# Kernel optimization log

Hardware: AMD Instinct MI355X
Metric: run time of the kernel (lower is better)

## Reference

```python
import jax, jax.numpy as jnp
import numpy as np

EPS = 1.1920929e-07  # torch clamp_probs eps for float32
TEMP = 0.3           # sampler temperature T


def conv1d(x, w, b, pad):
    # x: [B, Cin, L], w: [Cout, Cin, K] -> [B, Cout, L']
    y = jax.lax.conv_general_dilated(x, w, window_strides=(1,), padding=[(pad, pad)],
                                     dimension_numbers=('NCH', 'OIH', 'NCH'))
    return y + b[None, :, None]


def setup_inputs() -> dict:
    key = jax.random.key(0)
    ks = jax.random.split(key, 20)
    B, L, V, E, F, H, K = 512, 512, 100000, 100, 100, 100, 10
    p = lambda i, shape: jax.random.normal(ks[i], shape, jnp.float32) * 0.02
    return {
        'x': jax.random.randint(ks[0], (B, L), 0, V, dtype=jnp.int32),
        'u': jax.random.uniform(ks[1], (B, K, L), dtype=jnp.float32),
        'emb': p(2, (V, E)),
        'conv1_w': p(3, (F, E, 3)), 'conv1_b': p(4, (F,)),
        'gi_w': p(5, (H, F)), 'gi_b': p(6, (H,)),
        'conv2_w': p(7, (H, F, 3)), 'conv2_b': p(8, (H,)),
        'li_w': p(9, (H, H, 3)), 'li_b': p(10, (H,)),
        'conv3_w': p(11, (F, 2 * H, 1)), 'conv3_b': p(12, (F,)),
        'conv4_w': p(13, (1, F, 1)), 'conv4_b': p(14, (1,)),
        'fc1_w': p(15, (H, E)), 'fc1_b': p(16, (H,)),
        'head_w': p(17, (1, H)), 'head_b': p(18, (1,)),
    }


def _ti_logits(e, conv1_w, conv1_b, gi_w, gi_b, conv2_w, conv2_b,
               li_w, li_b, conv3_w, conv3_b, conv4_w, conv4_b):
    relu = jax.nn.relu
    xt = jnp.swapaxes(e, 1, 2)                       # [B, E, L]
    h = relu(conv1d(xt, conv1_w, conv1_b, 1))        # [B, F, L]
    g = relu(h.mean(axis=-1) @ gi_w.T + gi_b)        # [B, H] (AdaptiveAvgPool1d(1))
    loc = relu(conv1d(relu(conv1d(h, conv2_w, conv2_b, 1)), li_w, li_b, 1))  # [B, H, L]
    gexp = jnp.broadcast_to(g[:, :, None], loc.shape)
    z = jnp.concatenate([gexp, loc], axis=1)         # [B, 2H, L]
    z = relu(conv1d(z, conv3_w, conv3_b, 0))
    return conv1d(z, conv4_w, conv4_b, 0)            # [B, 1, L]


def reference(x, u, emb, conv1_w, conv1_b, gi_w, gi_b, conv2_w, conv2_b,
              li_w, li_b, conv3_w, conv3_b, conv4_w, conv4_b,
              fc1_w, fc1_b, head_w, head_b):
    e = emb[x]                                       # [B, L, E] embedding gather
    logits = _ti_logits(e, conv1_w, conv1_b, gi_w, gi_b, conv2_w, conv2_b,
                        li_w, li_b, conv3_w, conv3_b, conv4_w, conv4_b)
    # Gumbel top-k continuous sampling (training path)
    uc = jnp.clip(u, EPS, 1.0 - EPS)
    gumbel = -jnp.log(-jnp.log(uc))                  # [B, K, L]
    noisy = (gumbel + logits) / TEMP                 # logits [B,1,L] broadcasts over K
    csamples = jax.nn.softmax(noisy, axis=-1).max(axis=1)  # [B, L]
    # distil predictor: masked mean pooling + MLP + sigmoid head
    pooled = (e * csamples[:, :, None]).mean(axis=1)  # [B, E]
    h = jax.nn.relu(pooled @ fc1_w.T + fc1_b)
    out = jax.nn.sigmoid(h @ head_w.T + head_b)       # [B, 1]
    return out, csamples
```

## Files before the change

### kernel.cpp

```cpp
#include <hip/hip_runtime.h>
#include <math.h>

#define DEV __device__ __forceinline__

typedef __attribute__((ext_vector_type(8))) short short8;
typedef __attribute__((ext_vector_type(4))) short short4v;
typedef __attribute__((ext_vector_type(4))) float f32x4;

#define SSTR 136

DEV short f2bf(float f) {
    unsigned u = __builtin_bit_cast(unsigned, f);
    unsigned r = (u + 0x7fffu + ((u >> 16) & 1u)) >> 16;
    return (short)r;
}

__global__ __launch_bounds__(64) void pack_all_kernel(
    const float* __restrict__ c1w, const float* __restrict__ c2w,
    const float* __restrict__ liw, const float* __restrict__ c3w,
    short* __restrict__ A1, short* __restrict__ A2,
    short* __restrict__ A3, short* __restrict__ A4) {
    int bx = blockIdx.x;
    const float* w; short* dst; int mode, lbx;
    if (bx < 77)       { w = c1w; dst = A1; mode = 0; lbx = bx; }
    else if (bx < 154) { w = c2w; dst = A2; mode = 0; lbx = bx - 77; }
    else if (bx < 231) { w = liw; dst = A3; mode = 0; lbx = bx - 154; }
    else               { w = c3w; dst = A4; mode = 1; lbx = bx - 231; }
    int ks = lbx / 7, mt = lbx - ks * 7;
    int lane = threadIdx.x;
    int f = mt * 16 + (lane & 15);
    int kb = ks * 32 + (lane >> 4) * 8;
    short8 v;
#pragma unroll
    for (int j = 0; j < 8; ++j) {
        int kk = kb + j;
        float val = 0.f;
        if (f < 100) {
            if (mode == 0) {
                int dk = kk / 112, c = kk - dk * 112;
                if (dk < 3 && c < 100) val = w[(f * 100 + c) * 3 + dk];
            } else {
                if (kk < 100) val = w[f * 200 + 100 + kk];
            }
        }
        v[j] = f2bf(val);
    }
    *(short8*)&dst[(lbx * 64 + lane) * 8] = v;
}

template<int NT, bool POOL, bool TO_GLOBAL>
DEV void conv3tap(const short* __restrict__ Ap, const float* __restrict__ bias,
                  const short* s_src, short* s_dst, short* __restrict__ gout,
                  int row0l, int l0, float* __restrict__ hpart, int pbase,
                  int lane, int wv) {
    const int q = lane >> 4, n = lane & 15;
    const int mt0 = wv * 2;
    const bool two = (wv < 3);
    const f32x4 z4 = {0.f, 0.f, 0.f, 0.f};
    f32x4 acc0[NT], acc1[NT];
#pragma unroll
    for (int nt = 0; nt < NT; ++nt) { acc0[nt] = z4; acc1[nt] = z4; }
#pragma unroll
    for (int ks = 0; ks < 11; ++ks) {
        short8 a0 = *(const short8*)&Ap[(ks * 448 + mt0 * 64 + lane) * 8];
        short8 a1;
        if (two) a1 = *(const short8*)&Ap[(ks * 448 + (mt0 + 1) * 64 + lane) * 8];
        int oct = ks * 4 + q, dk, c0;
        if (oct >= 42) { dk = 0; c0 = 0; }
        else { dk = oct / 14; c0 = (oct - dk * 14) * 8; }
#pragma unroll
        for (int nt = 0; nt < NT; ++nt) {
            int r = nt * 16 + n + dk; if (r > 69) r = 69;
            short8 bf = *(const short8*)&s_src[r * SSTR + c0];
            acc0[nt] = __builtin_amdgcn_mfma_f32_16x16x32_bf16(a0, bf, acc0[nt], 0, 0, 0);
            if (two)
                acc1[nt] = __builtin_amdgcn_mfma_f32_16x16x32_bf16(a1, bf, acc1[nt], 0, 0, 0);
        }
    }
    const int fb0 = mt0 * 16 + q * 4;
    const int fb1 = fb0 + 16;
    f32x4 bs0 = (fb0 < 100) ? *(const f32x4*)&bias[fb0] : z4;
    f32x4 bs1 = (two && fb1 < 100) ? *(const f32x4*)&bias[fb1] : z4;
    f32x4 ps0 = z4, ps1 = z4;
#pragma unroll
    for (int nt = 0; nt < NT; ++nt) {
        const int j = nt * 16 + n;
        const int l = row0l + j;
        const bool lok = (l >= 0) && (l < 512);
        const bool pok = (l >= l0) && (l < l0 + 64);
        short4v pk0, pk1;
#pragma unroll
        for (int r = 0; r < 4; ++r) {
            float v0 = fmaxf(acc0[nt][r] + bs0[r], 0.f);
            v0 = lok ? v0 : 0.f;
            pk0[r] = f2bf(v0);
            if constexpr (POOL) { if (pok) ps0[r] += v0; }
            if (two) {
                float v1 = fmaxf(acc1[nt][r] + bs1[r], 0.f);
                v1 = lok ? v1 : 0.f;
                pk1[r] = f2bf(v1);
                if constexpr (POOL) { if (pok) ps1[r] += v1; }
            }
        }
        if constexpr (TO_GLOBAL) {
            if (j < 64) {
                *(short4v*)&gout[j * 112 + fb0] = pk0;
                if (two) *(short4v*)&gout[j * 112 + fb1] = pk1;
            }
        } else {
            if (j < 70) {
                *(short4v*)&s_dst[j * SSTR + fb0] = pk0;
                if (two) *(short4v*)&s_dst[j * SSTR + fb1] = pk1;
            }
        }
    }
    if constexpr (POOL) {
#pragma unroll
        for (int off = 1; off <= 8; off <<= 1)
#pragma unroll
            for (int r = 0; r < 4; ++r) {
                ps0[r] += __shfl_xor(ps0[r], off, 64);
                ps1[r] += __shfl_xor(ps1[r], off, 64);
            }
        if (n == 0) {
            *(f32x4*)&hpart[pbase * 112 + fb0] = ps0;
            if (two) *(f32x4*)&hpart[pbase * 112 + fb1] = ps1;
        }
    }
}

__global__ __launch_bounds__(256, 4) void fused_conv_kernel(
    const int* __restrict__ xidx, const float* __restrict__ emb,
    const short* __restrict__ A1, const short* __restrict__ A2,
    const short* __restrict__ A3,
    const float* __restrict__ b1, const float* __restrict__ b2,
    const float* __restrict__ b3,
    short* __restrict__ locT, float* __restrict__ hpart) {
    extern __shared__ char smem[];
    short* s_e = (short*)smem;
    short* s_h = (short*)(smem + 72 * SSTR * 2);
    const int tid = threadIdx.x;
    const int b = blockIdx.y, bx = blockIdx.x, l0 = bx * 64;
    const int lane = tid & 63, wv = tid >> 6;

#pragma unroll
    for (int idx = tid; idx < 70 * 28; idx += 256) {
        int j = idx / 28, c4 = idx - j * 28;
        int lg = l0 - 3 + j;
        short4v v = {0, 0, 0, 0};
        if (c4 < 25) {
            if (lg >= 0 && lg < 512) {
                int row = xidx[b * 512 + lg];
                f32x4 ev = *(const f32x4*)&emb[row * 100 + c4 * 4];
#pragma unroll
                for (int r = 0; r < 4; ++r) v[r] = f2bf(ev[r]);
            }
        }
        *(short4v*)&s_e[j * SSTR + c4 * 4] = v;
    }
    __syncthreads();
    conv3tap<5, true, false>(A1, b1, s_e, s_h, nullptr, l0 - 2, l0,
                             hpart, b * 8 + bx, lane, wv);
    __syncthreads();
    conv3tap<5, false, false>(A2, b2, s_h, s_e, nullptr, l0 - 1, l0,
                              nullptr, 0, lane, wv);
    __syncthreads();
    conv3tap<4, false, true>(A3, b3, s_e, nullptr,
                             locT + ((size_t)b * 512 + l0) * 112, l0, l0,
                             nullptr, 0, lane, wv);
}

__global__ __launch_bounds__(256, 4) void conv3_logits_kernel(
    const short* __restrict__ locT, const short* __restrict__ A4,
    const float* __restrict__ zg, const float* __restrict__ w4,
    const float* __restrict__ b4, float* __restrict__ logits) {
    extern __shared__ char smem[];
    short* s_in = (short*)smem;
    float* s_part = (float*)(smem + 128 * SSTR * 2);
    const int tid = threadIdx.x;
    const int b = blockIdx.y, l0r = blockIdx.x * 128;
    const int lane = tid & 63, wv = tid >> 6;
    const int q = lane >> 4, n = lane & 15;

    {
        short8 tmp[7];
#pragma unroll
        for (int p = 0; p < 7; ++p) {
            int idx = tid + p * 256;
            int j = idx / 14, c8 = idx - j * 14;
            tmp[p] = *(const short8*)&locT[((size_t)b * 512 + l0r + j) * 112 + c8 * 8];
        }
#pragma unroll
        for (int p = 0; p < 7; ++p) {
            int idx = tid + p * 256;
            int j = idx / 14, c8 = idx - j * 14;
            *(short8*)&s_in[j * SSTR + c8 * 8] = tmp[p];
        }
    }
    __syncthreads();

    const f32x4 z4 = {0.f, 0.f, 0.f, 0.f};
    const int mt0 = wv * 2;
    const bool two = (wv < 3);
    f32x4 acc0[8], acc1[8];
#pragma unroll
    for (int nt = 0; nt < 8; ++nt) { acc0[nt] = z4; acc1[nt] = z4; }
#pragma unroll
    for (int ks = 0; ks < 4; ++ks) {
        short8 a0 = *(const short8*)&A4[(ks * 448 + mt0 * 64 + lane) * 8];
        short8 a1;
        if (two) a1 = *(const short8*)&A4[(ks * 448 + (mt0 + 1) * 64 + lane) * 8];
        int c0 = (ks * 4 + q) * 8;
        if (c0 > 104) c0 = 104;
#pragma unroll
        for (int nt = 0; nt < 8; ++nt) {
            short8 bf = *(const short8*)&s_in[(nt * 16 + n) * SSTR + c0];
            acc0[nt] = __builtin_amdgcn_mfma_f32_16x16x32_bf16(a0, bf, acc0[nt], 0, 0, 0);
            if (two)
                acc1[nt] = __builtin_amdgcn_mfma_f32_16x16x32_bf16(a1, bf, acc1[nt], 0, 0, 0);
        }
    }
    const int fb0 = mt0 * 16 + q * 4, fb1 = fb0 + 16;
    f32x4 w40 = (fb0 < 100) ? *(const f32x4*)&w4[fb0] : z4;
    f32x4 w41 = (two && fb1 < 100) ? *(const f32x4*)&w4[fb1] : z4;
    f32x4 zg0 = *(const f32x4*)&zg[b * 112 + fb0];
    f32x4 zg1 = two ? *(const f32x4*)&zg[b * 112 + fb1] : z4;
#pragma unroll
    for (int nt = 0; nt < 8; ++nt) {
        float part = 0.f;
#pragma unroll
        for (int r = 0; r < 4; ++r) {
            part += fmaxf(acc0[nt][r] + zg0[r], 0.f) * w40[r];
            if (two) part += fmaxf(acc1[nt][r] + zg1[r], 0.f) * w41[r];
        }
        part += __shfl_xor(part, 16, 64);
        part += __shfl_xor(part, 32, 64);
        if (q == 0) s_part[wv * 128 + nt * 16 + n] = part;
    }
    __syncthreads();
    if (tid < 128) {
        float s = s_part[tid] + s_part[128 + tid] + s_part[256 + tid] +
                  s_part[384 + tid] + b4[0];
        logits[b * 512 + l0r + tid] = s;
    }
}

__global__ __launch_bounds__(128) void pool_gate_kernel(
    const float* __restrict__ hpart, const float* __restrict__ gi_w,
    const float* __restrict__ gi_b, const float* __restrict__ w3,
    const float* __restrict__ b3, float* __restrict__ zg) {
    int b = blockIdx.x, tid = threadIdx.x;
    __shared__ float s_hm[112];
    __shared__ float s_g[100];
    if (tid < 112) {
        float a = 0.f;
#pragma unroll
        for (int s = 0; s < 8; ++s) a += hpart[(b * 8 + s) * 112 + tid];
        s_hm[tid] = a * (1.f / 512.f);
    }
    __syncthreads();
    if (tid < 100) {
        float a = gi_b[tid];
        for (int f = 0; f < 100; ++f) a += s_hm[f] * gi_w[tid * 100 + f];
        s_g[tid] = fmaxf(a, 0.f);
    }
    __syncthreads();
    if (tid < 112) {
        float a = 0.f;
        if (tid < 100) {
            a = b3[tid];
            for (int h = 0; h < 100; ++h) a += s_g[h] * w3[tid * 200 + h];
        }
        zg[b * 112 + tid] = a;
    }
}

__global__ __launch_bounds__(256) void sampler_kernel(
    const float* __restrict__ u, const float* __restrict__ logits,
    float* __restrict__ cs) {
    const float EPSV = 1.1920929e-07f;
    int b = blockIdx.x, tid = threadIdx.x;
    int lane = tid & 63, wv = tid >> 6;
    __shared__ float s_log[512], s_cs[512], s_red[8];
    float uu[20];
#pragma unroll
    for (int k = 0; k < 10; ++k) {
        uu[k * 2]     = u[(b * 10 + k) * 512 + tid];
        uu[k * 2 + 1] = u[(b * 10 + k) * 512 + tid + 256];
    }
    for (int l = tid; l < 512; l += 256) { s_log[l] = logits[b * 512 + l]; s_cs[l] = 0.f; }
    __syncthreads();
    for (int k = 0; k < 10; ++k) {
        float nz[2];
#pragma unroll
        for (int i = 0; i < 2; ++i) {
            int l = tid + i * 256;
            float vv = fminf(fmaxf(uu[k * 2 + i], EPSV), 1.f - EPSV);
            float g = -__logf(-__logf(vv));
            nz[i] = (g + s_log[l]) * (1.f / 0.3f);
        }
        float m = fmaxf(nz[0], nz[1]);
#pragma unroll
        for (int off = 32; off >= 1; off >>= 1) m = fmaxf(m, __shfl_xor(m, off, 64));
        if (lane == 0) s_red[wv] = m;
        __syncthreads();
        m = fmaxf(fmaxf(s_red[0], s_red[1]), fmaxf(s_red[2], s_red[3]));
        float e0 = __expf(nz[0] - m), e1 = __expf(nz[1] - m);
        float s = e0 + e1;
#pragma unroll
        for (int off = 32; off >= 1; off >>= 1) s += __shfl_xor(s, off, 64);
        if (lane == 0) s_red[4 + wv] = s;
        __syncthreads();
        float inv = 1.f / (s_red[4] + s_red[5] + s_red[6] + s_red[7]);
        s_cs[tid]       = fmaxf(s_cs[tid],       e0 * inv);
        s_cs[tid + 256] = fmaxf(s_cs[tid + 256], e1 * inv);
    }
    for (int l = tid; l < 512; l += 256) cs[b * 512 + l] = s_cs[l];
}

__global__ __launch_bounds__(256) void head_part_kernel(
    const int* __restrict__ xidx, const float* __restrict__ emb,
    const float* __restrict__ cs, float* __restrict__ hp) {
    int sb = blockIdx.x, b = blockIdx.y;
    int tid = threadIdx.x;
    __shared__ int s_x[64];
    __shared__ float s_c[64];
    __shared__ float s_acc[8][104];
    if (tid < 64) {
        int l = sb * 64 + tid;
        s_x[tid] = xidx[b * 512 + l];
        s_c[tid] = cs[b * 512 + l];
    }
    __syncthreads();
    int s = tid & 31, lq = tid >> 5;
    if (s < 25) {
        f32x4 a = {0.f, 0.f, 0.f, 0.f};
#pragma unroll
        for (int i = 0; i < 8; ++i) {
            int ll = lq * 8 + i;
            int row = s_x[ll];
            float cv = s_c[ll];
            f32x4 ev = *(const f32x4*)&emb[row * 100 + s * 4];
#pragma unroll
            for (int r = 0; r < 4; ++r) a[r] += ev[r] * cv;
        }
        *(f32x4*)&s_acc[lq][s * 4] = a;
    }
    __syncthreads();
    if (tid < 100) {
        float v = 0.f;
#pragma unroll
        for (int j = 0; j < 8; ++j) v += s_acc[j][tid];
        hp[(b * 8 + sb) * 100 + tid] = v;
    }
}

__global__ __launch_bounds__(128) void head_fin_kernel(
    const float* __restrict__ hp, const float* __restrict__ fc1_w,
    const float* __restrict__ fc1_b, const float* __restrict__ head_w,
    const float* __restrict__ head_b, float* __restrict__ out) {
    int b = blockIdx.x, tid = threadIdx.x;
    int lane = tid & 63, wv = tid >> 6;
    __shared__ float s_pool[100];
    __shared__ float s_h2[100];
    __shared__ float s_red[2];
    if (tid < 100) {
        float a = 0.f;
#pragma unroll
        for (int sb = 0; sb < 8; ++sb) a += hp[(b * 8 + sb) * 100 + tid];
        s_pool[tid] = a * (1.f / 512.f);
    }
    __syncthreads();
    if (tid < 100) {
        float acc = fc1_b[tid];
        for (int i = 0; i < 100; ++i) acc += s_pool[i] * fc1_w[tid * 100 + i];
        s_h2[tid] = fmaxf(acc, 0.f);
    }
    __syncthreads();
    float v = (tid < 100) ? s_h2[tid] * head_w[tid] : 0.f;
#pragma unroll
    for (int off = 32; off >= 1; off >>= 1) v += __shfl_xor(v, off, 64);
    if (lane == 0) s_red[wv] = v;
    __syncthreads();
    if (tid == 0) {
        float z = s_red[0] + s_red[1] + head_b[0];
        out[b] = 1.f / (1.f + __expf(-z));
    }
}

extern "C" void kernel_launch(void* const* d_in, const int* in_sizes, int n_in,
                              void* d_out, int out_size, void* d_ws, size_t ws_size,
                              hipStream_t stream) {
    const int*   x   = (const int*)d_in[0];
    const float* u   = (const float*)d_in[1];
    const float* emb = (const float*)d_in[2];
    const float* c1w = (const float*)d_in[3];
    const float* c1b = (const float*)d_in[4];
    const float* giw = (const float*)d_in[5];
    const float* gib = (const float*)d_in[6];
    const float* c2w = (const float*)d_in[7];
    const float* c2b = (const float*)d_in[8];
    const float* liw = (const float*)d_in[9];
    const float* lib = (const float*)d_in[10];
    const float* c3w = (const float*)d_in[11];
    const float* c3b = (const float*)d_in[12];
    const float* c4w = (const float*)d_in[13];
    const float* c4b = (const float*)d_in[14];
    const float* f1w = (const float*)d_in[15];
    const float* f1b = (const float*)d_in[16];
    const float* hww = (const float*)d_in[17];
    const float* hbb = (const float*)d_in[18];
    float* out = (float*)d_out;

    char* ws = (char*)d_ws;
    short* locT   = (short*)(ws + 0);
    short* A1     = (short*)(ws + 58720256);
    short* A2     = (short*)(ws + 58799104);
    short* A3     = (short*)(ws + 58877952);
    short* A4     = (short*)(ws + 58956800);
    float* zg     = (float*)(ws + 58985472);
    float* logits = (float*)(ws + 59214848);
    float* hpart  = (float*)(ws + 60263424);
    float* hp     = (float*)(ws + 62098432);

    pack_all_kernel<<<259, 64, 0, stream>>>(c1w, c2w, liw, c3w, A1, A2, A3, A4);

    size_t smemA = 2 * 72 * SSTR * 2;
    fused_conv_kernel<<<dim3(8, 512), 256, smemA, stream>>>(
        x, emb, A1, A2, A3, c1b, c2b, lib, locT, hpart);
    pool_gate_kernel<<<512, 128, 0, stream>>>(hpart, giw, gib, c3w, c3b, zg);
    size_t smemB = 128 * SSTR * 2 + 4 * 128 * 4;
    conv3_logits_kernel<<<dim3(4, 512), 256, smemB, stream>>>(
        locT, A4, zg, c4w, c4b, logits);
    sampler_kernel<<<512, 256, 0, stream>>>(u, logits, out + 512);
    head_part_kernel<<<dim3(8, 512), 256, 0, stream>>>(x, emb, out + 512, hp);
    head_fin_kernel<<<512, 128, 0, stream>>>(hp, f1w, f1b, hww, hbb, out);
}
```

Before: 289.2 us.

## Pre-convert embedding table to padded bf16 and tighten conv K packing

A new kernel converts the full fp32 embedding table into a bf16 table padded to 112 columns on every call. The fused conv kernel then gathers 16-byte bf16 rows directly instead of converting fp32 per tile. The 3-tap conv weights are repacked to 13 channel-octets per tap, which cuts the MFMA K loop from 11 to 10 steps, and LDS B-operand addressing is hoisted into a base pointer. The trade-off is a full read of the table and about 22 MB of bf16 writes per call, in exchange for roughly halving the traffic of the gather.

```diff
diff --git a/kernel.cpp b/kernel.cpp
--- a/kernel.cpp
+++ b/kernel.cpp
@@ -13,6 +13,21 @@
     unsigned u = __builtin_bit_cast(unsigned, f);
     unsigned r = (u + 0x7fffu + ((u >> 16) & 1u)) >> 16;
     return (short)r;
+}
+
+__global__ __launch_bounds__(256) void emb_cvt_kernel(
+    const float* __restrict__ emb, short* __restrict__ embT) {
+    int t = threadIdx.x;
+    int row = blockIdx.x * 8 + (t >> 5);
+    int c4 = t & 31;
+    if (c4 >= 28) return;
+    short4v v = {0, 0, 0, 0};
+    if (c4 < 25) {
+        f32x4 e = *(const f32x4*)&emb[row * 100 + c4 * 4];
+#pragma unroll
+        for (int r = 0; r < 4; ++r) v[r] = f2bf(e[r]);
+    }
+    *(short4v*)&embT[row * 112 + c4 * 4] = v;
 }
 
 __global__ __launch_bounds__(64) void pack_all_kernel(
@@ -22,14 +37,13 @@
     short* __restrict__ A3, short* __restrict__ A4) {
     int bx = blockIdx.x;
     const float* w; short* dst; int mode, lbx;
-    if (bx < 77)       { w = c1w; dst = A1; mode = 0; lbx = bx; }
-    else if (bx < 154) { w = c2w; dst = A2; mode = 0; lbx = bx - 77; }
-    else if (bx < 231) { w = liw; dst = A3; mode = 0; lbx = bx - 154; }
-    else               { w = c3w; dst = A4; mode = 1; lbx = bx - 231; }
-    int ks = lbx / 7, mt = lbx - ks * 7;
+    if (bx < 70)       { w = c1w; dst = A1; mode = 0; lbx = bx; }
+    else if (bx < 140) { w = c2w; dst = A2; mode = 0; lbx = bx - 70; }
+    else if (bx < 210) { w = liw; dst = A3; mode = 0; lbx = bx - 140; }
+    else               { w = c3w; dst = A4; mode = 1; lbx = bx - 210; }
     int lane = threadIdx.x;
-    int f = mt * 16 + (lane & 15);
-    int kb = ks * 32 + (lane >> 4) * 8;
+    int f = lbx % 7 * 16 + (lane & 15);
+    int kb = (lbx / 7) * 32 + (lane >> 4) * 8;
     short8 v;
 #pragma unroll
     for (int j = 0; j < 8; ++j) {
@@ -37,7 +51,8 @@
         float val = 0.f;
         if (f < 100) {
             if (mode == 0) {
-                int dk = kk / 112, c = kk - dk * 112;
+                int oct = kk >> 3, dk = oct / 13;
+                int c = (oct - 13 * dk) * 8 + (kk & 7);
                 if (dk < 3 && c < 100) val = w[(f * 100 + c) * 3 + dk];
             } else {
                 if (kk < 100) val = w[f * 200 + 100 + kk];
@@ -61,17 +76,23 @@
 #pragma unroll
     for (int nt = 0; nt < NT; ++nt) { acc0[nt] = z4; acc1[nt] = z4; }
 #pragma unroll
-    for (int ks = 0; ks < 11; ++ks) {
+    for (int ks = 0; ks < 10; ++ks) {
         short8 a0 = *(const short8*)&Ap[(ks * 448 + mt0 * 64 + lane) * 8];
         short8 a1;
         if (two) a1 = *(const short8*)&Ap[(ks * 448 + (mt0 + 1) * 64 + lane) * 8];
-        int oct = ks * 4 + q, dk, c0;
-        if (oct >= 42) { dk = 0; c0 = 0; }
-        else { dk = oct / 14; c0 = (oct - dk * 14) * 8; }
+        int oct = ks * 4 + q;
+        int dk = oct / 13;
+        int c0 = (oct - 13 * dk) * 8;
+        const short* bptr = s_src + (n + dk) * SSTR + c0;
 #pragma unroll
         for (int nt = 0; nt < NT; ++nt) {
-            int r = nt * 16 + n + dk; if (r > 69) r = 69;
-            short8 bf = *(const short8*)&s_src[r * SSTR + c0];
+            short8 bf;
+            if (nt < 4) {
+                bf = *(const short8*)(bptr + nt * 16 * SSTR);
+            } else {
+                int r = 64 + n + dk; if (r > 69) r = 69;
+                bf = *(const short8*)&s_src[r * SSTR + c0];
+            }
             acc0[nt] = __builtin_amdgcn_mfma_f32_16x16x32_bf16(a0, bf, acc0[nt], 0, 0, 0);
             if (two)
                 acc1[nt] = __builtin_amdgcn_mfma_f32_16x16x32_bf16(a1, bf, acc1[nt], 0, 0, 0);
@@ -130,7 +151,7 @@
 }
 
 __global__ __launch_bounds__(256, 4) void fused_conv_kernel(
-    const int* __restrict__ xidx, const float* __restrict__ emb,
+    const int* __restrict__ xidx, const short* __restrict__ embT,
     const short* __restrict__ A1, const short* __restrict__ A2,
     const short* __restrict__ A3,
     const float* __restrict__ b1, const float* __restrict__ b2,
@@ -144,19 +165,18 @@
     const int lane = tid & 63, wv = tid >> 6;
 
 #pragma unroll
-    for (int idx = tid; idx < 70 * 28; idx += 256) {
-        int j = idx / 28, c4 = idx - j * 28;
-        int lg = l0 - 3 + j;
-        short4v v = {0, 0, 0, 0};
-        if (c4 < 25) {
+    for (int p = 0; p < 5; ++p) {
+        int idx = tid + p * 256;
+        int j = idx >> 4, c8 = idx & 15;
+        if (j < 70 && c8 < 14) {
+            int lg = l0 - 3 + j;
+            short8 v = {0, 0, 0, 0, 0, 0, 0, 0};
             if (lg >= 0 && lg < 512) {
                 int row = xidx[b * 512 + lg];
-                f32x4 ev = *(const f32x4*)&emb[row * 100 + c4 * 4];
-#pragma unroll
-                for (int r = 0; r < 4; ++r) v[r] = f2bf(ev[r]);
-            }
-        }
-        *(short4v*)&s_e[j * SSTR + c4 * 4] = v;
+                v = *(const short8*)&embT[row * 112 + c8 * 8];
+            }
+            *(short8*)&s_e[j * SSTR + c8 * 8] = v;
+        }
     }
     __syncthreads();
     conv3tap<5, true, false>(A1, b1, s_e, s_h, nullptr, l0 - 2, l0,
@@ -183,18 +203,20 @@
     const int q = lane >> 4, n = lane & 15;
 
     {
-        short8 tmp[7];
-#pragma unroll
-        for (int p = 0; p < 7; ++p) {
+        short8 tmp[8];
+#pragma unroll
+        for (int p = 0; p < 8; ++p) {
             int idx = tid + p * 256;
-            int j = idx / 14, c8 = idx - j * 14;
-            tmp[p] = *(const short8*)&locT[((size_t)b * 512 + l0r + j) * 112 + c8 * 8];
-        }
-#pragma unroll
-        for (int p = 0; p < 7; ++p) {
+            int j = idx >> 4, c8 = idx & 15;
+            if (c8 < 14)
+                tmp[p] = *(const short8*)&locT[((size_t)b * 512 + l0r + j) * 112 + c8 * 8];
+        }
+#pragma unroll
+        for (int p = 0; p < 8; ++p) {
             int idx = tid + p * 256;
-            int j = idx / 14, c8 = idx - j * 14;
-            *(short8*)&s_in[j * SSTR + c8 * 8] = tmp[p];
+            int j = idx >> 4, c8 = idx & 15;
+            if (c8 < 14)
+                *(short8*)&s_in[j * SSTR + c8 * 8] = tmp[p];
         }
     }
     __syncthreads();
@@ -212,9 +234,10 @@
         if (two) a1 = *(const short8*)&A4[(ks * 448 + (mt0 + 1) * 64 + lane) * 8];
         int c0 = (ks * 4 + q) * 8;
         if (c0 > 104) c0 = 104;
+        const short* bptr = s_in + n * SSTR + c0;
 #pragma unroll
         for (int nt = 0; nt < 8; ++nt) {
-            short8 bf = *(const short8*)&s_in[(nt * 16 + n) * SSTR + c0];
+            short8 bf = *(const short8*)(bptr + nt * 16 * SSTR);
             acc0[nt] = __builtin_amdgcn_mfma_f32_16x16x32_bf16(a0, bf, acc0[nt], 0, 0, 0);
             if (two)
                 acc1[nt] = __builtin_amdgcn_mfma_f32_16x16x32_bf16(a1, bf, acc1[nt], 0, 0, 0);
@@ -414,20 +437,22 @@
 
     char* ws = (char*)d_ws;
     short* locT   = (short*)(ws + 0);
-    short* A1     = (short*)(ws + 58720256);
-    short* A2     = (short*)(ws + 58799104);
-    short* A3     = (short*)(ws + 58877952);
-    short* A4     = (short*)(ws + 58956800);
-    float* zg     = (float*)(ws + 58985472);
-    float* logits = (float*)(ws + 59214848);
-    float* hpart  = (float*)(ws + 60263424);
-    float* hp     = (float*)(ws + 62098432);
-
-    pack_all_kernel<<<259, 64, 0, stream>>>(c1w, c2w, liw, c3w, A1, A2, A3, A4);
+    short* embT   = (short*)(ws + 58720256);
+    short* A1     = (short*)(ws + 81120256);
+    short* A2     = (short*)(ws + 81191936);
+    short* A3     = (short*)(ws + 81263616);
+    short* A4     = (short*)(ws + 81335296);
+    float* zg     = (float*)(ws + 81363968);
+    float* logits = (float*)(ws + 81593344);
+    float* hpart  = (float*)(ws + 82641920);
+    float* hp     = (float*)(ws + 84476928);
+
+    emb_cvt_kernel<<<12500, 256, 0, stream>>>(emb, embT);
+    pack_all_kernel<<<238, 64, 0, stream>>>(c1w, c2w, liw, c3w, A1, A2, A3, A4);
 
     size_t smemA = 2 * 72 * SSTR * 2;
     fused_conv_kernel<<<dim3(8, 512), 256, smemA, stream>>>(
-        x, emb, A1, A2, A3, c1b, c2b, lib, locT, hpart);
+        x, embT, A1, A2, A3, c1b, c2b, lib, locT, hpart);
     pool_gate_kernel<<<512, 128, 0, stream>>>(hpart, giw, gib, c3w, c3b, zg);
     size_t smemB = 128 * SSTR * 2 + 4 * 128 * 4;
     conv3_logits_kernel<<<dim3(4, 512), 256, smemB, stream>>>(
```

Measured after the change: 288.1 us. About the same (-0.4%).
